# Kernel optimization log

Measured on AMD Instinct MI355X. Metric: run time of the kernel, lower is better.

## Reference

```python
import jax, jax.numpy as jnp
import numpy as np

N_NODES = 100000
N_EDGES = 1600000
IN_FEATS = 16
H_FEAT = 128
NUM_CLASSES = 4
N_HIDDEN_LAYERS = 19  # layers 2..20 (128->128)
NEG_SLOPE = 0.01      # torch nn.LeakyReLU default


def setup_inputs() -> dict:
    key = jax.random.key(0)
    ks = jax.random.split(key, 10)
    node_feat = jax.random.normal(ks[0], (N_NODES, IN_FEATS), dtype=jnp.float32)
    edge_weight = jax.random.uniform(ks[1], (N_EDGES,), dtype=jnp.float32)
    src = jax.random.randint(ks[2], (N_EDGES,), 0, N_NODES, dtype=jnp.int32)
    dst = jax.random.randint(ks[3], (N_EDGES,), 0, N_NODES, dtype=jnp.int32)
    # Glorot-ish init for GraphConv weights, zero biases (DGL default)
    W1 = jax.random.normal(ks[4], (IN_FEATS, H_FEAT), dtype=jnp.float32) * (1.0 / np.sqrt(IN_FEATS))
    b1 = jnp.zeros((H_FEAT,), dtype=jnp.float32)
    W_stack = jax.random.normal(ks[5], (N_HIDDEN_LAYERS, H_FEAT, H_FEAT), dtype=jnp.float32) * (1.0 / np.sqrt(H_FEAT))
    b_stack = jnp.zeros((N_HIDDEN_LAYERS, H_FEAT), dtype=jnp.float32)
    fc_W = jax.random.normal(ks[6], (H_FEAT, NUM_CLASSES), dtype=jnp.float32) * (1.0 / np.sqrt(H_FEAT))
    fc_b = jnp.zeros((NUM_CLASSES,), dtype=jnp.float32)
    return {"node_feat": node_feat, "edge_weight": edge_weight, "src": src, "dst": dst,
            "W1": W1, "b1": b1, "W_stack": W_stack, "b_stack": b_stack,
            "fc_W": fc_W, "fc_b": fc_b}


def _degree_norms(src, dst, n_nodes, dtype):
    ones = jnp.ones(src.shape, dtype=dtype)
    out_deg = jax.ops.segment_sum(ones, src, num_segments=n_nodes)
    in_deg = jax.ops.segment_sum(ones, dst, num_segments=n_nodes)
    # DGL clamps degrees to min 1 for norm='both'
    inv_sqrt_out = jax.lax.rsqrt(jnp.maximum(out_deg, 1.0))
    inv_sqrt_in = jax.lax.rsqrt(jnp.maximum(in_deg, 1.0))
    return inv_sqrt_out, inv_sqrt_in


def _graph_conv(h, W, b, src, dst, ew, inv_sqrt_out, inv_sqrt_in, n_nodes):
    # DGL GraphConv norm='both' with edge_weight: u_mul_e message, sum at dst
    hs = h * inv_sqrt_out[:, None]                     # [N, F] src-side norm
    m = hs[src] * ew[:, None]                          # [E, F] edge messages
    agg = jax.ops.segment_sum(m, dst, num_segments=n_nodes)  # [N, F]
    agg = agg * inv_sqrt_in[:, None]                   # dst-side norm
    return agg @ W + b


def reference(node_feat, edge_weight, src, dst, W1, b1, W_stack, b_stack, fc_W, fc_b):
    n_nodes = node_feat.shape[0]
    iso, isi = _degree_norms(src, dst, n_nodes, node_feat.dtype)
    leaky = lambda x: jnp.where(x >= 0, x, NEG_SLOPE * x)

    h = leaky(_graph_conv(node_feat, W1, b1, src, dst, edge_weight, iso, isi, n_nodes))

    def body(h, wb):
        W, b = wb
        h = leaky(_graph_conv(h, W, b, src, dst, edge_weight, iso, isi, n_nodes))
        return h, None

    h, _ = jax.lax.scan(body, h, (W_stack, b_stack))
    return h @ fc_W + fc_b
```

## Files before the change

### kernel.cpp

```cpp
#include <hip/hip_runtime.h>

#define NN 100000
#define NE 1600000
#define HF 128
#define INF 16
#define NLAYERS 19
#define NB_SCAN 98

static inline int idiv(int a, int b) { return (a + b - 1) / b; }

__device__ __forceinline__ float leaky(float v) { return (v >= 0.f) ? v : 0.01f * v; }


__global__ __launch_bounds__(256) void k_deg1(const int* __restrict__ idx, int* __restrict__ deg,
                                              int e0, int e1) {
  int i = e0 + (blockIdx.x * 256 + threadIdx.x) * 4;
  if (i + 4 <= e1) {
    int4 v = *reinterpret_cast<const int4*>(idx + i);
    atomicAdd(&deg[v.x], 1);
    atomicAdd(&deg[v.y], 1);
    atomicAdd(&deg[v.z], 1);
    atomicAdd(&deg[v.w], 1);
  } else {
    for (; i < e1; ++i) atomicAdd(&deg[idx[i]], 1);
  }
}

__global__ __launch_bounds__(256) void k_norms(const int* __restrict__ dout, const int* __restrict__ din,
                                               float* __restrict__ iso, float* __restrict__ isi, int n) {
  int i = blockIdx.x * 256 + threadIdx.x;
  if (i < n) {
    iso[i] = rsqrtf((float)(dout[i] > 1 ? dout[i] : 1));
    isi[i] = rsqrtf((float)(din[i] > 1 ? din[i] : 1));
  }
}


__global__ __launch_bounds__(1024) void k_scan_part(const int* __restrict__ cnt, int* __restrict__ bsum, int n) {
  __shared__ int wsum[16];
  const int tid = threadIdx.x;
  const int lane = tid & 63;
  const int wid = tid >> 6;
  int i = blockIdx.x * 1024 + tid;
  int v = (i < n) ? cnt[i] : 0;
  int s = v;
#pragma unroll
  for (int m = 1; m < 64; m <<= 1) s += __shfl_xor(s, m, 64);
  if (lane == 0) wsum[wid] = s;
  __syncthreads();
  if (tid == 0) {
    int t = 0;
#pragma unroll
    for (int j = 0; j < 16; j++) t += wsum[j];
    bsum[blockIdx.x] = t;
  }
}

__global__ __launch_bounds__(128) void k_scan_small(const int* __restrict__ bsum, int* __restrict__ boff,
                                                    int* __restrict__ rp, int n, int nb) {
  __shared__ int ws[2];
  const int tid = threadIdx.x;
  const int lane = tid & 63;
  const int wid = tid >> 6;
  int v = (tid < nb) ? bsum[tid] : 0;
  int x = v;
#pragma unroll
  for (int off = 1; off < 64; off <<= 1) {
    int t = __shfl_up(x, off, 64);
    if (lane >= off) x += t;
  }
  if (lane == 63) ws[wid] = x;
  __syncthreads();
  int add = (wid > 0) ? ws[0] : 0;
  if (tid < nb) boff[tid] = add + x - v;
  if (tid == 127) rp[n] = ws[0] + x;
}

__global__ __launch_bounds__(1024) void k_scan_final(const int* __restrict__ cnt, const int* __restrict__ boff,
                                                     int* __restrict__ rp, int n) {
  __shared__ int wsum[16];
  const int tid = threadIdx.x;
  const int lane = tid & 63;
  const int wid = tid >> 6;
  int i = blockIdx.x * 1024 + tid;
  int v = (i < n) ? cnt[i] : 0;
  int x = v;
#pragma unroll
  for (int off = 1; off < 64; off <<= 1) {
    int t = __shfl_up(x, off, 64);
    if (lane >= off) x += t;
  }
  if (lane == 63) wsum[wid] = x;
  __syncthreads();
  if (wid == 0) {
    int s = (lane < 16) ? wsum[lane] : 0;
#pragma unroll
    for (int off = 1; off < 16; off <<= 1) {
      int t = __shfl_up(s, off, 64);
      if (lane >= off) s += t;
    }
    if (lane < 16) wsum[lane] = s;
  }
  __syncthreads();
  int woff = (wid > 0) ? wsum[wid - 1] : 0;
  if (i < n) rp[i] = boff[blockIdx.x] + woff + x - v;
}

__global__ __launch_bounds__(256) void k_build(const int* __restrict__ src, const int* __restrict__ dst,
                                               const float* __restrict__ ew, const float* __restrict__ iso,
                                               const float* __restrict__ isi, const int* __restrict__ rp,
                                               int* __restrict__ cursor, int2* __restrict__ cv,
                                               int e0, int e1) {
  int i = e0 + blockIdx.x * 256 + threadIdx.x;
  if (i < e1) {
    int s = src[i], d = dst[i];
    int pos = rp[d] + atomicAdd(&cursor[d], 1);
    float v = ew[i] * iso[s] * isi[d];
    cv[pos] = make_int2(s, __float_as_int(v));
  }
}


__global__ __launch_bounds__(256) void k_spmm16(const float* __restrict__ x, const int* __restrict__ rp,
                                                const int2* __restrict__ cv, float* __restrict__ agg16, int n) {
  int t = blockIdx.x * 256 + threadIdx.x;
  int node = t >> 4, f = t & 15;
  if (node >= n) return;
  int e = rp[node], end = rp[node + 1];
  float a = 0.f;
  for (; e + 4 <= end; e += 4) {
    int2 q0 = cv[e], q1 = cv[e + 1], q2 = cv[e + 2], q3 = cv[e + 3];
    float x0 = x[(size_t)q0.x * INF + f];
    float x1 = x[(size_t)q1.x * INF + f];
    float x2 = x[(size_t)q2.x * INF + f];
    float x3 = x[(size_t)q3.x * INF + f];
    a = fmaf(__int_as_float(q0.y), x0, a);
    a = fmaf(__int_as_float(q1.y), x1, a);
    a = fmaf(__int_as_float(q2.y), x2, a);
    a = fmaf(__int_as_float(q3.y), x3, a);
  }
  for (; e < end; ++e) {
    int2 q = cv[e];
    a = fmaf(__int_as_float(q.y), x[(size_t)q.x * INF + f], a);
  }
  agg16[(size_t)node * INF + f] = a;
}

__global__ __launch_bounds__(256) void k_gemm16(const float* __restrict__ agg16, const float* __restrict__ W1,
                                                const float* __restrict__ b1, float* __restrict__ h, int n) {
  __shared__ float W1s[INF * HF];
  int tid = threadIdx.x;
  {
    float4* d4 = reinterpret_cast<float4*>(W1s);
    const float4* s4 = reinterpret_cast<const float4*>(W1);
    d4[tid] = s4[tid];
    d4[tid + 256] = s4[tid + 256];
  }
  __syncthreads();
  int t = blockIdx.x * 256 + tid;
  int node = t >> 7, c = t & 127;
  if (node >= n) return;
  const float* ar = agg16 + (size_t)node * INF;
  float4 a0 = *reinterpret_cast<const float4*>(ar);
  float4 a1 = *reinterpret_cast<const float4*>(ar + 4);
  float4 a2 = *reinterpret_cast<const float4*>(ar + 8);
  float4 a3 = *reinterpret_cast<const float4*>(ar + 12);
  float av[16] = {a0.x, a0.y, a0.z, a0.w, a1.x, a1.y, a1.z, a1.w,
                  a2.x, a2.y, a2.z, a2.w, a3.x, a3.y, a3.z, a3.w};
  float a = b1[c];
#pragma unroll
  for (int f = 0; f < INF; ++f) a = fmaf(av[f], W1s[f * HF + c], a);
  h[(size_t)t] = leaky(a);
}


__global__ __launch_bounds__(256) void k_spmm(const float* __restrict__ h, const int* __restrict__ rp,
                                              const int2* __restrict__ cv, float* __restrict__ agg, int n) {
  const int lane = threadIdx.x & 63;
  const int node = __builtin_amdgcn_readfirstlane(blockIdx.x * 4 + (threadIdx.x >> 6));
  if (node >= n) return;
  const int beg = rp[node], end = rp[node + 1];
  const size_t fo = (size_t)(lane << 1);
  float ax = 0.f, ay = 0.f;
  int e = beg;
  for (; e + 8 <= end; e += 8) {
    int2 q0 = cv[e + 0], q1 = cv[e + 1], q2 = cv[e + 2], q3 = cv[e + 3];
    int2 q4 = cv[e + 4], q5 = cv[e + 5], q6 = cv[e + 6], q7 = cv[e + 7];
    float2 x0 = *reinterpret_cast<const float2*>(h + (size_t)q0.x * HF + fo);
    float2 x1 = *reinterpret_cast<const float2*>(h + (size_t)q1.x * HF + fo);
    float2 x2 = *reinterpret_cast<const float2*>(h + (size_t)q2.x * HF + fo);
    float2 x3 = *reinterpret_cast<const float2*>(h + (size_t)q3.x * HF + fo);
    float2 x4 = *reinterpret_cast<const float2*>(h + (size_t)q4.x * HF + fo);
    float2 x5 = *reinterpret_cast<const float2*>(h + (size_t)q5.x * HF + fo);
    float2 x6 = *reinterpret_cast<const float2*>(h + (size_t)q6.x * HF + fo);
    float2 x7 = *reinterpret_cast<const float2*>(h + (size_t)q7.x * HF + fo);
    ax = fmaf(__int_as_float(q0.y), x0.x, ax); ay = fmaf(__int_as_float(q0.y), x0.y, ay);
    ax = fmaf(__int_as_float(q1.y), x1.x, ax); ay = fmaf(__int_as_float(q1.y), x1.y, ay);
    ax = fmaf(__int_as_float(q2.y), x2.x, ax); ay = fmaf(__int_as_float(q2.y), x2.y, ay);
    ax = fmaf(__int_as_float(q3.y), x3.x, ax); ay = fmaf(__int_as_float(q3.y), x3.y, ay);
    ax = fmaf(__int_as_float(q4.y), x4.x, ax); ay = fmaf(__int_as_float(q4.y), x4.y, ay);
    ax = fmaf(__int_as_float(q5.y), x5.x, ax); ay = fmaf(__int_as_float(q5.y), x5.y, ay);
    ax = fmaf(__int_as_float(q6.y), x6.x, ax); ay = fmaf(__int_as_float(q6.y), x6.y, ay);
    ax = fmaf(__int_as_float(q7.y), x7.x, ax); ay = fmaf(__int_as_float(q7.y), x7.y, ay);
  }
  if (e + 4 <= end) {
    int2 q0 = cv[e + 0], q1 = cv[e + 1], q2 = cv[e + 2], q3 = cv[e + 3];
    float2 x0 = *reinterpret_cast<const float2*>(h + (size_t)q0.x * HF + fo);
    float2 x1 = *reinterpret_cast<const float2*>(h + (size_t)q1.x * HF + fo);
    float2 x2 = *reinterpret_cast<const float2*>(h + (size_t)q2.x * HF + fo);
    float2 x3 = *reinterpret_cast<const float2*>(h + (size_t)q3.x * HF + fo);
    ax = fmaf(__int_as_float(q0.y), x0.x, ax); ay = fmaf(__int_as_float(q0.y), x0.y, ay);
    ax = fmaf(__int_as_float(q1.y), x1.x, ax); ay = fmaf(__int_as_float(q1.y), x1.y, ay);
    ax = fmaf(__int_as_float(q2.y), x2.x, ax); ay = fmaf(__int_as_float(q2.y), x2.y, ay);
    ax = fmaf(__int_as_float(q3.y), x3.x, ax); ay = fmaf(__int_as_float(q3.y), x3.y, ay);
    e += 4;
  }
  if (e + 2 <= end) {
    int2 q0 = cv[e + 0], q1 = cv[e + 1];
    float2 x0 = *reinterpret_cast<const float2*>(h + (size_t)q0.x * HF + fo);
    float2 x1 = *reinterpret_cast<const float2*>(h + (size_t)q1.x * HF + fo);
    ax = fmaf(__int_as_float(q0.y), x0.x, ax); ay = fmaf(__int_as_float(q0.y), x0.y, ay);
    ax = fmaf(__int_as_float(q1.y), x1.x, ax); ay = fmaf(__int_as_float(q1.y), x1.y, ay);
    e += 2;
  }
  if (e < end) {
    int2 q0 = cv[e];
    float2 x0 = *reinterpret_cast<const float2*>(h + (size_t)q0.x * HF + fo);
    ax = fmaf(__int_as_float(q0.y), x0.x, ax); ay = fmaf(__int_as_float(q0.y), x0.y, ay);
  }
  *reinterpret_cast<float2*>(agg + (size_t)node * HF + fo) = make_float2(ax, ay);
}

__global__ __launch_bounds__(256, 6) void k_gemm(const float* __restrict__ A, const float* __restrict__ W,
                                                 const float* __restrict__ bias, float* __restrict__ out, int n) {
  __shared__ float As[32][66];
  __shared__ float Ws[32][132];
  const int tid = threadIdx.x;
  const int n0 = blockIdx.x * 64;
  const int ty = tid >> 4;
  const int tx = tid & 15;
  float acc[4][8];
#pragma unroll
  for (int i = 0; i < 4; i++)
#pragma unroll
    for (int j = 0; j < 8; j++) acc[i][j] = 0.f;

  for (int kc = 0; kc < HF; kc += 32) {
    {
      int node = tid >> 2;
      int ng = n0 + node;
#pragma unroll
      for (int i = 0; i < 2; ++i) {
        int kq = ((tid & 3) * 2 + i) * 4;
        float4 v = make_float4(0.f, 0.f, 0.f, 0.f);
        if (ng < n) v = *reinterpret_cast<const float4*>(A + (size_t)ng * HF + kc + kq);
        As[kq + 0][node] = v.x;
        As[kq + 1][node] = v.y;
        As[kq + 2][node] = v.z;
        As[kq + 3][node] = v.w;
      }
    }
    {
      int c4 = (tid & 31) * 4;
      int r = tid >> 5;
#pragma unroll
      for (int p = 0; p < 4; ++p) {
        int rr = r + p * 8;
        *reinterpret_cast<float4*>(&Ws[rr][c4]) =
            *reinterpret_cast<const float4*>(W + (size_t)(kc + rr) * HF + c4);
      }
    }
    __syncthreads();
#pragma unroll
    for (int k = 0; k < 32; ++k) {
      float2 p0 = *reinterpret_cast<const float2*>(&As[k][ty * 4]);
      float2 p1 = *reinterpret_cast<const float2*>(&As[k][ty * 4 + 2]);
      float4 w0 = *reinterpret_cast<const float4*>(&Ws[k][tx * 4]);
      float4 w1 = *reinterpret_cast<const float4*>(&Ws[k][tx * 4 + 64]);
      float av[4] = {p0.x, p0.y, p1.x, p1.y};
      float wv[8] = {w0.x, w0.y, w0.z, w0.w, w1.x, w1.y, w1.z, w1.w};
#pragma unroll
      for (int i = 0; i < 4; i++)
#pragma unroll
        for (int j = 0; j < 8; j++) acc[i][j] = fmaf(av[i], wv[j], acc[i][j]);
    }
    __syncthreads();
  }

  float4 bb0 = *reinterpret_cast<const float4*>(bias + tx * 4);
  float4 bb1 = *reinterpret_cast<const float4*>(bias + tx * 4 + 64);
  float bb[8] = {bb0.x, bb0.y, bb0.z, bb0.w, bb1.x, bb1.y, bb1.z, bb1.w};
#pragma unroll
  for (int i = 0; i < 4; ++i) {
    int node = n0 + ty * 4 + i;
    if (node < n) {
      float o[8];
#pragma unroll
      for (int j = 0; j < 8; j++) o[j] = leaky(acc[i][j] + bb[j]);
      *reinterpret_cast<float4*>(out + (size_t)node * HF + tx * 4) = make_float4(o[0], o[1], o[2], o[3]);
      *reinterpret_cast<float4*>(out + (size_t)node * HF + tx * 4 + 64) = make_float4(o[4], o[5], o[6], o[7]);
    }
  }
}


__global__ __launch_bounds__(256) void k_head(const float* __restrict__ h, const float* __restrict__ fcW,
                                              const float* __restrict__ fcb, float* __restrict__ out, int n) {
  int gw = (blockIdx.x * 256 + threadIdx.x) >> 6;
  int lane = threadIdx.x & 63;
  int node = gw * 8 + (lane >> 3);
  int part = lane & 7;
  float a0 = 0.f, a1 = 0.f, a2 = 0.f, a3 = 0.f;
  if (node < n) {
    const float* hp = h + (size_t)node * HF + part * 16;
#pragma unroll
    for (int i = 0; i < 16; i++) {
      float xv = hp[i];
      float4 wk = *reinterpret_cast<const float4*>(fcW + (part * 16 + i) * 4);
      a0 = fmaf(xv, wk.x, a0);
      a1 = fmaf(xv, wk.y, a1);
      a2 = fmaf(xv, wk.z, a2);
      a3 = fmaf(xv, wk.w, a3);
    }
  }
#pragma unroll
  for (int m = 1; m < 8; m <<= 1) {
    a0 += __shfl_xor(a0, m, 64);
    a1 += __shfl_xor(a1, m, 64);
    a2 += __shfl_xor(a2, m, 64);
    a3 += __shfl_xor(a3, m, 64);
  }
  if (part == 0 && node < n) {
    float4 o = make_float4(a0 + fcb[0], a1 + fcb[1], a2 + fcb[2], a3 + fcb[3]);
    *reinterpret_cast<float4*>(out + (size_t)node * 4) = o;
  }
}


extern "C" void kernel_launch(void* const* d_in, const int* in_sizes, int n_in,
                              void* d_out, int out_size, void* d_ws, size_t ws_size,
                              hipStream_t stream) {
  const float* x = (const float*)d_in[0];
  const float* ew = (const float*)d_in[1];
  const int* src = (const int*)d_in[2];
  const int* dst = (const int*)d_in[3];
  const float* W1 = (const float*)d_in[4];
  const float* b1 = (const float*)d_in[5];
  const float* Wst = (const float*)d_in[6];
  const float* bst = (const float*)d_in[7];
  const float* fcW = (const float*)d_in[8];
  const float* fcb = (const float*)d_in[9];
  float* out = (float*)d_out;

  const int n = NN, e = NE;
  char* w = (char*)d_ws;
  size_t off = 0;
  auto alloc = [&](size_t bytes) {
    void* p = w + off;
    off += (bytes + 511) & ~(size_t)511;
    return p;
  };
  int* dout = (int*)alloc((size_t)n * 4);
  int* din = (int*)alloc((size_t)n * 4);
  float* iso = (float*)alloc((size_t)n * 4);
  float* isi = (float*)alloc((size_t)n * 4);
  int* rp = (int*)alloc((size_t)(n + 1) * 4);
  int* cursor = (int*)alloc((size_t)n * 4);
  int* bsum = (int*)alloc((size_t)NB_SCAN * 4);
  int* boff = (int*)alloc((size_t)NB_SCAN * 4);
  int2* cv = (int2*)alloc((size_t)e * 8);
  float* h = (float*)alloc((size_t)n * HF * 4);
  float* agg = (float*)alloc((size_t)n * HF * 4);
  float* agg16 = agg;

  hipMemsetAsync(dout, 0, (size_t)n * 4, stream);
  hipMemsetAsync(din, 0, (size_t)n * 4, stream);
  hipMemsetAsync(cursor, 0, (size_t)n * 4, stream);

  const int eh = 800000;
  k_deg1<<<idiv(eh, 1024), 256, 0, stream>>>(src, dout, 0, eh);
  k_deg1<<<idiv(e - eh, 1024), 256, 0, stream>>>(src, dout, eh, e);
  k_deg1<<<idiv(eh, 1024), 256, 0, stream>>>(dst, din, 0, eh);
  k_deg1<<<idiv(e - eh, 1024), 256, 0, stream>>>(dst, din, eh, e);
  k_norms<<<idiv(n, 256), 256, 0, stream>>>(dout, din, iso, isi, n);

  k_scan_part<<<NB_SCAN, 1024, 0, stream>>>(din, bsum, n);
  k_scan_small<<<1, 128, 0, stream>>>(bsum, boff, rp, n, NB_SCAN);
  k_scan_final<<<NB_SCAN, 1024, 0, stream>>>(din, boff, rp, n);

  k_build<<<idiv(eh, 256), 256, 0, stream>>>(src, dst, ew, iso, isi, rp, cursor, cv, 0, eh);
  k_build<<<idiv(e - eh, 256), 256, 0, stream>>>(src, dst, ew, iso, isi, rp, cursor, cv, eh, e);

  k_spmm16<<<idiv(n * INF, 256), 256, 0, stream>>>(x, rp, cv, agg16, n);
  k_gemm16<<<idiv(n * HF, 256), 256, 0, stream>>>(agg16, W1, b1, h, n);

  for (int l = 0; l < NLAYERS; ++l) {
    k_spmm<<<idiv(n, 4), 256, 0, stream>>>(h, rp, cv, agg, n);
    k_gemm<<<idiv(n, 64), 256, 0, stream>>>(agg, Wst + (size_t)l * HF * HF, bst + (size_t)l * HF, h, n);
  }
  k_head<<<idiv(n * 8, 256), 256, 0, stream>>>(h, fcW, fcb, out, n);
}
```

Before: 3.406 ms.

## Replace FP32 hidden-layer GEMM with split-bf16 MFMA emulating FP32 precision

Each hidden-layer weight matrix is pre-split once into three bf16 parts in an MFMA-friendly layout. The 128x128 dense transform then runs on bf16 MFMA instructions with six cross products, so FP32 accuracy is approximately kept. Activations are split on the fly per K-chunk. The aim is to cut the FP32 FMA cost of the GEMM in each of the 19 layers, at the price of extra split arithmetic, a small preprocessing kernel and scalar rather than vectorized output stores.

After: 3.240 ms (median of 2 runs). 1.05x faster.

```diff
diff --git a/kernel.cpp b/kernel.cpp
--- a/kernel.cpp
+++ b/kernel.cpp
@@ -10,6 +10,21 @@
 static inline int idiv(int a, int b) { return (a + b - 1) / b; }
 
 __device__ __forceinline__ float leaky(float v) { return (v >= 0.f) ? v : 0.01f * v; }
+
+typedef __attribute__((ext_vector_type(8))) __bf16 bf16x8;
+typedef __attribute__((ext_vector_type(4))) float f32x4;
+
+__device__ __forceinline__ unsigned short rne_bf16(float x) {
+  unsigned int u = __float_as_uint(x);
+  unsigned int r = (u + 0x7fffu + ((u >> 16) & 1u)) >> 16;
+  return (unsigned short)r;
+}
+__device__ __forceinline__ float bf2f(unsigned short h) {
+  return __uint_as_float(((unsigned int)h) << 16);
+}
+__device__ __forceinline__ __bf16 bfbits(unsigned short h) {
+  return __builtin_bit_cast(__bf16, h);
+}
 
 
 __global__ __launch_bounds__(256) void k_deg1(const int* __restrict__ idx, int* __restrict__ deg,
@@ -118,6 +133,40 @@
     float v = ew[i] * iso[s] * isi[d];
     cv[pos] = make_int2(s, __float_as_int(v));
   }
+}
+
+__global__ __launch_bounds__(256) void k_wsplit(const float* __restrict__ Wst, unsigned short* __restrict__ W3,
+                                                int nlayers) {
+  int g = blockIdx.x * 256 + threadIdx.x;
+  int lane = g & 63;
+  int fid = g >> 6;
+  if (fid >= nlayers * 32) return;
+  int layer = fid >> 5;
+  int rem = fid & 31;
+  int kc = rem >> 3;
+  int t8 = rem & 7;
+  const float* W = Wst + (size_t)layer * HF * HF;
+  int col = t8 * 16 + (lane & 15);
+  int krow = kc * 32 + (lane >> 4) * 8;
+  unsigned int o1[4], o2[4], o3[4];
+#pragma unroll
+  for (int i = 0; i < 4; ++i) {
+    float xa = W[(size_t)(krow + 2 * i) * HF + col];
+    float xb = W[(size_t)(krow + 2 * i + 1) * HF + col];
+    unsigned short a1 = rne_bf16(xa); float ra1 = xa - bf2f(a1);
+    unsigned short a2 = rne_bf16(ra1); float ra2 = ra1 - bf2f(a2);
+    unsigned short a3 = rne_bf16(ra2);
+    unsigned short b1 = rne_bf16(xb); float rb1 = xb - bf2f(b1);
+    unsigned short b2 = rne_bf16(rb1); float rb2 = rb1 - bf2f(b2);
+    unsigned short b3 = rne_bf16(rb2);
+    o1[i] = (unsigned)a1 | ((unsigned)b1 << 16);
+    o2[i] = (unsigned)a2 | ((unsigned)b2 << 16);
+    o3[i] = (unsigned)a3 | ((unsigned)b3 << 16);
+  }
+  size_t base = (size_t)layer * 49152 + (size_t)kc * 4096 + (size_t)t8 * 512 + (size_t)lane * 8;
+  *reinterpret_cast<uint4*>(W3 + base)         = make_uint4(o1[0], o1[1], o1[2], o1[3]);
+  *reinterpret_cast<uint4*>(W3 + base + 16384) = make_uint4(o2[0], o2[1], o2[2], o2[3]);
+  *reinterpret_cast<uint4*>(W3 + base + 32768) = make_uint4(o3[0], o3[1], o3[2], o3[3]);
 }
 
 
@@ -231,74 +280,83 @@
   *reinterpret_cast<float2*>(agg + (size_t)node * HF + fo) = make_float2(ax, ay);
 }
 
-__global__ __launch_bounds__(256, 6) void k_gemm(const float* __restrict__ A, const float* __restrict__ W,
-                                                 const float* __restrict__ bias, float* __restrict__ out, int n) {
-  __shared__ float As[32][66];
-  __shared__ float Ws[32][132];
+__global__ __launch_bounds__(256) void k_mfma(const float* __restrict__ A, const unsigned short* __restrict__ W3L,
+                                              const float* __restrict__ bias, float* __restrict__ out, int n) {
+  __shared__ unsigned short WB[3 * 4096];
   const int tid = threadIdx.x;
+  const int w = tid >> 6;
+  const int l = tid & 63;
   const int n0 = blockIdx.x * 64;
-  const int ty = tid >> 4;
-  const int tx = tid & 15;
-  float acc[4][8];
-#pragma unroll
-  for (int i = 0; i < 4; i++)
-#pragma unroll
-    for (int j = 0; j < 8; j++) acc[i][j] = 0.f;
-
-  for (int kc = 0; kc < HF; kc += 32) {
+  const int m15 = l & 15;
+  const int g4 = l >> 4;
+
+  const int nodeA = n0 + w * 16 + m15;
+  const bool aok = nodeA < n;
+  const float* ap = A + (size_t)nodeA * HF + g4 * 8;
+
+  f32x4 acc[8];
+#pragma unroll
+  for (int t = 0; t < 8; ++t) acc[t] = (f32x4){0.f, 0.f, 0.f, 0.f};
+
+  float4* WB4 = reinterpret_cast<float4*>(WB);
+  const float4* G4 = reinterpret_cast<const float4*>(W3L);
+
+  for (int kc = 0; kc < 4; ++kc) {
+    float4 fA = make_float4(0.f, 0.f, 0.f, 0.f);
+    float4 fB = make_float4(0.f, 0.f, 0.f, 0.f);
+    if (aok) {
+      fA = *reinterpret_cast<const float4*>(ap + kc * 32);
+      fB = *reinterpret_cast<const float4*>(ap + kc * 32 + 4);
+    }
+#pragma unroll
+    for (int s = 0; s < 6; ++s) {
+      int lin = s * 256 + tid;
+      int p = lin >> 9;
+      int off = lin & 511;
+      WB4[lin] = G4[(p * 4 + kc) * 512 + off];
+    }
+    __syncthreads();
+    bf16x8 fa1, fa2, fa3;
     {
-      int node = tid >> 2;
-      int ng = n0 + node;
-#pragma unroll
-      for (int i = 0; i < 2; ++i) {
-        int kq = ((tid & 3) * 2 + i) * 4;
-        float4 v = make_float4(0.f, 0.f, 0.f, 0.f);
-        if (ng < n) v = *reinterpret_cast<const float4*>(A + (size_t)ng * HF + kc + kq);
-        As[kq + 0][node] = v.x;
-        As[kq + 1][node] = v.y;
-        As[kq + 2][node] = v.z;
-        As[kq + 3][node] = v.w;
+      float xs[8] = {fA.x, fA.y, fA.z, fA.w, fB.x, fB.y, fB.z, fB.w};
+#pragma unroll
+      for (int i = 0; i < 8; ++i) {
+        float x = xs[i];
+        unsigned short h1 = rne_bf16(x);
+        float r1 = x - bf2f(h1);
+        unsigned short h2 = rne_bf16(r1);
+        float r2 = r1 - bf2f(h2);
+        unsigned short h3 = rne_bf16(r2);
+        fa1[i] = bfbits(h1);
+        fa2[i] = bfbits(h2);
+        fa3[i] = bfbits(h3);
       }
     }
-    {
-      int c4 = (tid & 31) * 4;
-      int r = tid >> 5;
-#pragma unroll
-      for (int p = 0; p < 4; ++p) {
-        int rr = r + p * 8;
-        *reinterpret_cast<float4*>(&Ws[rr][c4]) =
-            *reinterpret_cast<const float4*>(W + (size_t)(kc + rr) * HF + c4);
-      }
+    const bf16x8* WBv = reinterpret_cast<const bf16x8*>(WB);
+#pragma unroll
+    for (int t = 0; t < 8; ++t) {
+      bf16x8 b1 = WBv[t * 64 + l];
+      bf16x8 b2 = WBv[512 + t * 64 + l];
+      bf16x8 b3 = WBv[1024 + t * 64 + l];
+      acc[t] = __builtin_amdgcn_mfma_f32_16x16x32_bf16(fa1, b1, acc[t], 0, 0, 0);
+      acc[t] = __builtin_amdgcn_mfma_f32_16x16x32_bf16(fa1, b2, acc[t], 0, 0, 0);
+      acc[t] = __builtin_amdgcn_mfma_f32_16x16x32_bf16(fa2, b1, acc[t], 0, 0, 0);
+      acc[t] = __builtin_amdgcn_mfma_f32_16x16x32_bf16(fa2, b2, acc[t], 0, 0, 0);
+      acc[t] = __builtin_amdgcn_mfma_f32_16x16x32_bf16(fa1, b3, acc[t], 0, 0, 0);
+      acc[t] = __builtin_amdgcn_mfma_f32_16x16x32_bf16(fa3, b1, acc[t], 0, 0, 0);
     }
     __syncthreads();
-#pragma unroll
-    for (int k = 0; k < 32; ++k) {
-      float2 p0 = *reinterpret_cast<const float2*>(&As[k][ty * 4]);
-      float2 p1 = *reinterpret_cast<const float2*>(&As[k][ty * 4 + 2]);
-      float4 w0 = *reinterpret_cast<const float4*>(&Ws[k][tx * 4]);
-      float4 w1 = *reinterpret_cast<const float4*>(&Ws[k][tx * 4 + 64]);
-      float av[4] = {p0.x, p0.y, p1.x, p1.y};
-      float wv[8] = {w0.x, w0.y, w0.z, w0.w, w1.x, w1.y, w1.z, w1.w};
-#pragma unroll
-      for (int i = 0; i < 4; i++)
-#pragma unroll
-        for (int j = 0; j < 8; j++) acc[i][j] = fmaf(av[i], wv[j], acc[i][j]);
-    }
-    __syncthreads();
-  }
-
-  float4 bb0 = *reinterpret_cast<const float4*>(bias + tx * 4);
-  float4 bb1 = *reinterpret_cast<const float4*>(bias + tx * 4 + 64);
-  float bb[8] = {bb0.x, bb0.y, bb0.z, bb0.w, bb1.x, bb1.y, bb1.z, bb1.w};
-#pragma unroll
-  for (int i = 0; i < 4; ++i) {
-    int node = n0 + ty * 4 + i;
-    if (node < n) {
-      float o[8];
-#pragma unroll
-      for (int j = 0; j < 8; j++) o[j] = leaky(acc[i][j] + bb[j]);
-      *reinterpret_cast<float4*>(out + (size_t)node * HF + tx * 4) = make_float4(o[0], o[1], o[2], o[3]);
-      *reinterpret_cast<float4*>(out + (size_t)node * HF + tx * 4 + 64) = make_float4(o[4], o[5], o[6], o[7]);
+  }
+
+  const int baserow = n0 + w * 16 + g4 * 4;
+#pragma unroll
+  for (int t = 0; t < 8; ++t) {
+    int col = t * 16 + m15;
+    float bb = bias[col];
+#pragma unroll
+    for (int r = 0; r < 4; ++r) {
+      int node = baserow + r;
+      if (node < n) out[(size_t)node * HF + col] = leaky(acc[t][r] + bb);
     }
   }
 }
@@ -368,6 +426,7 @@
   int* cursor = (int*)alloc((size_t)n * 4);
   int* bsum = (int*)alloc((size_t)NB_SCAN * 4);
   int* boff = (int*)alloc((size_t)NB_SCAN * 4);
+  unsigned short* W3 = (unsigned short*)alloc((size_t)NLAYERS * 49152 * 2);
   int2* cv = (int2*)alloc((size_t)e * 8);
   float* h = (float*)alloc((size_t)n * HF * 4);
   float* agg = (float*)alloc((size_t)n * HF * 4);
@@ -376,6 +435,8 @@
   hipMemsetAsync(dout, 0, (size_t)n * 4, stream);
   hipMemsetAsync(din, 0, (size_t)n * 4, stream);
   hipMemsetAsync(cursor, 0, (size_t)n * 4, stream);
+
+  k_wsplit<<<idiv(NLAYERS * 32 * 64, 256), 256, 0, stream>>>(Wst, W3, NLAYERS);
 
   const int eh = 800000;
   k_deg1<<<idiv(eh, 1024), 256, 0, stream>>>(src, dout, 0, eh);
@@ -396,7 +457,7 @@
 
   for (int l = 0; l < NLAYERS; ++l) {
     k_spmm<<<idiv(n, 4), 256, 0, stream>>>(h, rp, cv, agg, n);
-    k_gemm<<<idiv(n, 64), 256, 0, stream>>>(agg, Wst + (size_t)l * HF * HF, bst + (size_t)l * HF, h, n);
+    k_mfma<<<idiv(n, 64), 256, 0, stream>>>(agg, W3 + (size_t)l * 49152, bst + (size_t)l * HF, h, n);
   }
   k_head<<<idiv(n * 8, 256), 256, 0, stream>>>(h, fcW, fcb, out, n);
 }
```
